# Kernel tuning notes

Measured on AMD Instinct MI355X. Metric: run time of the kernel, lower is better.

Reference implementation:

```python
import jax, jax.numpy as jnp
import numpy as np

# static config (matches init_kwargs)
NH, NKV, E, K = 16, 4, 8, 2
CAP_FACTOR = 1.25
LN_EPS = 1e-5


def _layer_norm(x, w, b):
    mu = jnp.mean(x, axis=-1, keepdims=True)
    var = jnp.mean(jnp.square(x - mu), axis=-1, keepdims=True)
    return (x - mu) * jax.lax.rsqrt(var + LN_EPS) * w + b


def setup_inputs() -> dict:
    key = jax.random.key(0)
    ks = jax.random.split(key, 6)
    S, B, H, F = 2048, 1, 1024, 2048
    HD = H // NH
    qkv_out = NKV * ((NH // NKV) + 2) * HD  # 1536
    f32 = jnp.float32
    return {
        "hidden_states": jax.random.normal(ks[0], (S, B, H), f32),
        "ln1_weight": jnp.ones((H,), f32),
        "ln1_bias": jnp.zeros((H,), f32),
        "ln2_weight": jnp.ones((H,), f32),
        "ln2_bias": jnp.zeros((H,), f32),
        "qkv_weight": jax.random.normal(ks[1], (qkv_out, H), f32) * 0.02,
        "proj_weight": jax.random.normal(ks[2], (H, H), f32) * 0.02,
        "router_weight": jax.random.normal(ks[3], (H, E), f32) * 0.02,
        "moe_w1": jax.random.normal(ks[4], (E, H, F), f32) * 0.02,
        "moe_w2": jax.random.normal(ks[5], (F and E, F, H), f32)[:E] * 0.02 if False else jax.random.normal(ks[5], (E, F, H), f32) * 0.02,
    }


def reference(hidden_states, ln1_weight, ln1_bias, ln2_weight, ln2_bias,
              qkv_weight, proj_weight, router_weight, moe_w1, moe_w2):
    S, B, H = hidden_states.shape
    HD = H // NH
    q_per_kv = NH // NKV
    # ---- attention block (cp_size=1: all-to-alls are identity) ----
    ln1 = _layer_norm(hidden_states, ln1_weight, ln1_bias)
    qkv = jnp.einsum('sbh,oh->sbo', ln1, qkv_weight)
    qkv = qkv.reshape(S, B, NKV, (q_per_kv + 2) * HD)
    q = qkv[..., : q_per_kv * HD].reshape(S, B, NH, HD)
    k = qkv[..., q_per_kv * HD:(q_per_kv + 1) * HD]          # [S,B,NKV,HD]
    v = qkv[..., (q_per_kv + 1) * HD:]                        # [S,B,NKV,HD]
    qb = jnp.transpose(q, (1, 2, 0, 3)).reshape(B, NKV, q_per_kv, S, HD)
    kb = jnp.transpose(k, (1, 2, 0, 3))                       # [B,NKV,S,HD]
    vb = jnp.transpose(v, (1, 2, 0, 3))
    scale = 1.0 / np.sqrt(HD).astype(np.float32)
    scores = jnp.einsum('bgqsd,bgtd->bgqst', qb, kb) * scale  # [B,NKV,qpk,S,S]
    causal = jnp.tril(jnp.ones((S, S), bool))
    scores = jnp.where(causal, scores, jnp.finfo(scores.dtype).min)
    attn = jax.nn.softmax(scores, axis=-1)
    ao = jnp.einsum('bgqst,bgtd->bgqsd', attn, vb)
    ao = ao.reshape(B, NH, S, HD)
    ao = jnp.transpose(ao, (2, 0, 1, 3)).reshape(S, B, H)
    proj = jnp.einsum('sbh,oh->sbo', ao, proj_weight)
    h1 = hidden_states + proj
    # ---- MoE block (ep_size=1: uniform all-to-all is identity) ----
    ln2 = _layer_norm(h1, ln2_weight, ln2_bias)
    x = ln2.reshape(-1, H)                                    # [N,H]
    N = x.shape[0]
    logits = x @ router_weight                                # linear(x, router_weight.t())
    probs = jax.nn.softmax(logits, axis=-1)
    top_p, top_i = jax.lax.top_k(probs, K)
    top_p = top_p / jnp.sum(top_p, axis=-1, keepdims=True)
    exp_idx = top_i.reshape(-1)                               # [N*K]
    exp_p = top_p.reshape(-1)
    # stable sort by expert id, capacity-padded dispatch
    order = jnp.argsort(exp_idx, stable=True)
    sorted_exp = exp_idx[order]
    counts = jnp.bincount(exp_idx, length=E)
    offsets = jnp.concatenate([jnp.zeros((1,), counts.dtype), jnp.cumsum(counts)[:-1]])
    within = jnp.arange(N * K) - offsets[sorted_exp]
    cap = int(np.ceil(N * K / E * CAP_FACTOR))
    T = E * cap
    valid = within < cap
    dst = jnp.where(valid, sorted_exp * cap + within, T)      # T = out-of-bounds -> dropped
    padded_tokens = jnp.zeros((T, H), x.dtype).at[dst].set(x[order // K], mode='drop')
    padded_probs = jnp.zeros((T,), exp_p.dtype).at[dst].set(exp_p[order], mode='drop')
    padded_tid = jnp.zeros((T,), jnp.int32).at[dst].set((order // K).astype(jnp.int32), mode='drop')
    # grouped expert GEMMs: [E,cap,H] x [E,H,F] -> gelu -> [E,cap,H]
    xt = padded_tokens.reshape(E, cap, H)
    fc1 = jax.nn.gelu(jnp.einsum('ech,ehf->ecf', xt, moe_w1))
    fc2 = jnp.einsum('ecf,efh->ech', fc1, moe_w2).reshape(T, H)
    weighted = fc2 * padded_probs[:, None]                    # pad slots have prob 0
    moe_out = jnp.zeros((N, H), hidden_states.dtype).at[padded_tid].add(weighted)
    return h1 + moe_out.reshape(S, B, H)
```

## Files before the change

### kernel.cpp

```cpp
#include <hip/hip_runtime.h>
#include <hip/hip_bf16.h>
#include <stdint.h>

#define S_LEN 2048
#define HDIM  1024
#define NHEAD 16
#define NKVH  4
#define HEADD 64
#define QKV_O 1536
#define NEXP  8
#define TOPK  2
#define CAP   640
#define TCAP  (NEXP*CAP)
#define FDIM  2048
#define LOG2E 1.44269504088896f
#define NCHUNK 40

typedef __bf16 bf16x8 __attribute__((ext_vector_type(8)));
typedef float  f32x4  __attribute__((ext_vector_type(4)));
typedef unsigned int u32;
typedef u32 u32x4 __attribute__((ext_vector_type(4)));
typedef u32 u32x2 __attribute__((ext_vector_type(2)));
typedef unsigned short u16;
typedef u16 u16x8 __attribute__((ext_vector_type(8)));

__device__ __forceinline__ void gload16(const __bf16* g, __bf16* l) {
    __builtin_amdgcn_global_load_lds(
        (const __attribute__((address_space(1))) u32*)g,
        (__attribute__((address_space(3))) u32*)l, 16, 0, 0);
}

__device__ __constant__ const signed char c_strip[NCHUNK] =
    {0,1,2,3, 4,4, 5,5, 6,6, 7,7, 8,8,8, 9,9,9, 10,10,10, 11,11,11,
     12,12,12,12, 13,13,13,13, 14,14,14,14, 15,15,15,15};
__device__ __constant__ const signed char c_chunk[NCHUNK] =
    {0,0,0,0, 0,1, 0,1, 0,1, 0,1, 0,1,2, 0,1,2, 0,1,2, 0,1,2,
     0,1,2,3, 0,1,2,3, 0,1,2,3, 0,1,2,3};
__device__ __constant__ const signed char c_cbase[16] = {0,1,2,3,4,6,8,10,12,15,18,21,24,28,32,36};
__device__ __constant__ const signed char c_nch[16]   = {1,1,1,1,2,2,2,2,3,3,3,3,4,4,4,4};

__global__ __launch_bounds__(256)
void prep_kernel(const float* __restrict__ hidden, const float* __restrict__ ln1w,
                 const float* __restrict__ ln1bb, const float* __restrict__ qkvW,
                 const float* __restrict__ projW, __bf16* __restrict__ ln1o,
                 __bf16* __restrict__ projWb, __bf16* __restrict__ qkvWb) {
    const int b = blockIdx.x, tid = threadIdx.x;
    if (b < S_LEN) {
        __shared__ float red[256];
        const float* x = hidden + (size_t)b * HDIM;
        float xr[4];
        #pragma unroll
        for (int j = 0; j < 4; ++j) xr[j] = x[tid + 256*j];
        float s = xr[0] + xr[1] + xr[2] + xr[3];
        red[tid] = s; __syncthreads();
        for (int st = 128; st > 0; st >>= 1) { if (tid < st) red[tid] += red[tid+st]; __syncthreads(); }
        float mu = red[0] / HDIM; __syncthreads();
        float v = 0.f;
        #pragma unroll
        for (int j = 0; j < 4; ++j) { float d = xr[j]-mu; v += d*d; }
        red[tid] = v; __syncthreads();
        for (int st = 128; st > 0; st >>= 1) { if (tid < st) red[tid] += red[tid+st]; __syncthreads(); }
        float rstd = rsqrtf(red[0]/HDIM + 1e-5f);
        #pragma unroll
        for (int j = 0; j < 4; ++j) {
            int i = tid + 256*j;
            ln1o[(size_t)b*HDIM + i] = (__bf16)((xr[j]-mu)*rstd*ln1w[i] + ln1bb[i]);
        }
        return;
    }
    const float* src; __bf16* dst; int i;
    if (b < S_LEN + 768) { src = qkvW; dst = qkvWb; i = (b - S_LEN)*256 + tid; }
    else                 { src = projW; dst = projWb; i = (b - S_LEN - 768)*256 + tid; }
    const float4* s = (const float4*)src + (size_t)i*2;
    float4 a = s[0], b4 = s[1];
    __bf16 tmp[8] = {(__bf16)a.x,(__bf16)a.y,(__bf16)a.z,(__bf16)a.w,
                     (__bf16)b4.x,(__bf16)b4.y,(__bf16)b4.z,(__bf16)b4.w};
    *(u32x4*)(dst + (size_t)i*8) = *(u32x4*)tmp;
}

__global__ __launch_bounds__(256)
void transp2_kernel(const float* __restrict__ w1, const float* __restrict__ w2,
                    __bf16* __restrict__ w1t, __bf16* __restrict__ w2t) {
    __shared__ float t[64][65];
    const int b = blockIdx.x;
    const float* src; __bf16* dst; int K, N, n0, k0;
    if (b < 4096) {
        int e = b >> 9, rem = b & 511;
        K = HDIM; N = FDIM; n0 = (rem & 31) * 64; k0 = (rem >> 5) * 64;
        src = w1 + (size_t)e*K*N; dst = w1t + (size_t)e*K*N;
    } else {
        int bb = b - 4096; int e = bb >> 9, rem = bb & 511;
        K = FDIM; N = HDIM; n0 = (rem & 15) * 64; k0 = (rem >> 4) * 64;
        src = w2 + (size_t)e*K*N; dst = w2t + (size_t)e*K*N;
    }
    const int tid = threadIdx.x;
    const int r = tid >> 4, c4 = (tid & 15) * 4;
    #pragma unroll
    for (int i = 0; i < 4; ++i) {
        float4 v = *(const float4*)(src + (size_t)(k0 + r + 16*i)*N + n0 + c4);
        t[r+16*i][c4+0] = v.x; t[r+16*i][c4+1] = v.y;
        t[r+16*i][c4+2] = v.z; t[r+16*i][c4+3] = v.w;
    }
    __syncthreads();
    const int rn = tid >> 3, kc = (tid & 7) * 8;
    #pragma unroll
    for (int i = 0; i < 2; ++i) {
        int n = rn + 32*i;
        __bf16 tmp[8];
        #pragma unroll
        for (int j = 0; j < 8; ++j) tmp[j] = (__bf16)t[kc+j][n];
        *(u32x4*)(dst + (size_t)(n0+n)*K + k0 + kc) = *(u32x4*)tmp;
    }
}

template<int EPI>
__global__ __launch_bounds__(256)
void gemm_bf16_kernel(const __bf16* __restrict__ A, const __bf16* __restrict__ Bt,
                      const float* __restrict__ R, void* __restrict__ Cout,
                      int N, int K, long sA, long sB, long sC) {
    __shared__ __bf16 As[128*64];
    __shared__ __bf16 Bs[128*64];
    const int e = blockIdx.z;
    A  += (size_t)e * sA;
    Bt += (size_t)e * sB;
    const int m0 = blockIdx.y*128, n0 = blockIdx.x*128;
    const int tid = threadIdx.x;
    const int lane = tid & 63, w = tid >> 6;
    const int lr = lane & 15, lg = lane >> 4;
    const int wr = w >> 1, wc = w & 1;
    const int srow8 = lane >> 3, sg = lane & 7;
    f32x4 acc[4][4] = {};
    for (int k0 = 0; k0 < K; k0 += 64) {
        __syncthreads();
        #pragma unroll
        for (int i = 0; i < 4; ++i) {
            int row = 32*w + 8*i + srow8;
            int src_g = sg ^ (row & 7);
            gload16(A  + (size_t)(m0+row)*K + k0 + src_g*8,
                    (__bf16*)((char*)As + (32*w + 8*i)*128));
            gload16(Bt + (size_t)(n0+row)*K + k0 + src_g*8,
                    (__bf16*)((char*)Bs + (32*w + 8*i)*128));
        }
        __syncthreads();
        #pragma unroll
        for (int ks = 0; ks < 2; ++ks) {
            bf16x8 af[4], bfr[4];
            #pragma unroll
            for (int mi = 0; mi < 4; ++mi) {
                int row = wr*64 + mi*16 + lr;
                af[mi] = *(const bf16x8*)((const char*)As + ((row*128 + (lg+4*ks)*16) ^ ((row&7)<<4)));
            }
            #pragma unroll
            for (int ni = 0; ni < 4; ++ni) {
                int row = wc*64 + ni*16 + lr;
                bfr[ni] = *(const bf16x8*)((const char*)Bs + ((row*128 + (lg+4*ks)*16) ^ ((row&7)<<4)));
            }
            #pragma unroll
            for (int mi = 0; mi < 4; ++mi)
                #pragma unroll
                for (int ni = 0; ni < 4; ++ni)
                    acc[mi][ni] = __builtin_amdgcn_mfma_f32_16x16x32_bf16(af[mi], bfr[ni], acc[mi][ni], 0,0,0);
        }
    }
    #pragma unroll
    for (int mi = 0; mi < 4; ++mi) {
        #pragma unroll
        for (int ni = 0; ni < 4; ++ni) {
            #pragma unroll
            for (int r = 0; r < 4; ++r) {
                int row = m0 + wr*64 + mi*16 + lg*4 + r;
                int col = n0 + wc*64 + ni*16 + lr;
                float v = acc[mi][ni][r];
                if (EPI == 1) v += R[(size_t)row*N + col];
                if (EPI == 2) {
                    float t = 0.7978845608028654f * (v + 0.044715f*v*v*v);
                    v = 0.5f * v * (1.f + tanhf(t));
                }
                if (EPI == 2 || EPI == 3)
                    ((__bf16*)Cout)[(size_t)e*sC + (size_t)row*N + col] = (__bf16)v;
                else
                    ((float*)Cout)[(size_t)e*sC + (size_t)row*N + col] = v;
            }
        }
    }
}

__global__ __launch_bounds__(512)
void attn_part_kernel(const __bf16* __restrict__ qkv, float* __restrict__ partO,
                      float* __restrict__ partML) {
    const int cx = blockIdx.x;
    const int h  = blockIdx.y;
    const int hg = h >> 2, qi = h & 3;
    const int qb = c_strip[cx];
    const int t0 = 4 * c_chunk[cx];
    const int t1 = min(qb + 1, t0 + 4);
    const int q0 = qb * 128;
    const int tid  = threadIdx.x;
    const int w    = tid >> 6;
    const int lane = tid & 63;
    const int lr   = lane & 15;
    const int lg   = lane >> 4;

    __shared__ __attribute__((aligned(16))) __bf16 Kls[128*64];
    __shared__ __attribute__((aligned(16))) __bf16 Vls[64*128];
    __shared__ __attribute__((aligned(16))) __bf16 Pls[8][16*64];

    const int krow = tid >> 2, kc = (tid & 3) * 2;
    const int va = tid & 63,  dg  = tid >> 6;
    u32x4 kreg[2]; u16x8 vreg[2];

    const __bf16* kbase = qkv + hg*384 + 256;
    const __bf16* vbase = qkv + hg*384 + 320;

#define ISSUE(T) do { \
        const __bf16* kp = kbase + (size_t)((T)*128 + krow)*QKV_O + kc*8; \
        kreg[0] = *(const u32x4*)(kp); \
        kreg[1] = *(const u32x4*)(kp + 8); \
        const __bf16* vp = vbase + (size_t)((T)*128 + 2*va)*QKV_O + dg*8; \
        vreg[0] = *(const u16x8*)(vp); \
        vreg[1] = *(const u16x8*)(vp + QKV_O); \
    } while(0)

#define COMMIT() do { \
        char* Kb = (char*)Kls; \
        *(u32x4*)(Kb + ((krow*128 + (kc+0)*16) ^ ((krow&7)<<4))) = kreg[0]; \
        *(u32x4*)(Kb + ((krow*128 + (kc+1)*16) ^ ((krow&7)<<4))) = kreg[1]; \
        char* Vb = (char*)Vls; \
        _Pragma("unroll") \
        for (int j = 0; j < 8; ++j) { \
            int d = dg*8 + j; \
            u32 u = ((u32)vreg[1][j] << 16) | vreg[0][j]; \
            *(u32*)(Vb + ((d*256 + va*4) ^ ((d&7)<<4))) = u; \
        } \
    } while(0)

    const int qrow = q0 + w*16 + lr;
    const __bf16* qp = qkv + (size_t)qrow*QKV_O + hg*384 + qi*64;
    bf16x8 qfrag[2];
    #pragma unroll
    for (int ks = 0; ks < 2; ++ks) {
        bf16x8 qr = *(const bf16x8*)(qp + ks*32 + lg*8);
        #pragma unroll
        for (int j = 0; j < 8; ++j) qfrag[ks][j] = (__bf16)((float)qr[j] * 0.125f);
    }
    bf16x8 ones;
    #pragma unroll
    for (int j = 0; j < 8; ++j) ones[j] = (__bf16)1.0f;

    f32x4 oacc[4] = {};
    f32x4 lcol = {};
    float mrow[4] = {-INFINITY,-INFINITY,-INFINITY,-INFINITY};

    ISSUE(t0);
    for (int t = t0; t < t1; ++t) {
        __syncthreads();
        COMMIT();
        if (t+1 < t1) ISSUE(t+1);
        __syncthreads();

        f32x4 sacc[8] = {};
        const char* Kb = (const char*)Kls;
        #pragma unroll
        for (int f = 0; f < 8; ++f) {
            int row = lr + 16*f;
            int swz = (row & 7) << 4;
            #pragma unroll
            for (int ks = 0; ks < 2; ++ks) {
                bf16x8 kf = *(const bf16x8*)(Kb + ((row*128 + (lg*8+32*ks)*2) ^ swz));
                sacc[f] = __builtin_amdgcn_mfma_f32_16x16x32_bf16(qfrag[ks], kf, sacc[f], 0,0,0);
            }
        }
        if (t == qb) {
            #pragma unroll
            for (int f = 0; f < 8; ++f)
                #pragma unroll
                for (int r = 0; r < 4; ++r)
                    if (lr + 16*f > 16*w + 4*lg + r) sacc[f][r] = -INFINITY;
        }
        float tm[4];
        #pragma unroll
        for (int r = 0; r < 4; ++r) {
            float a = fmaxf(fmaxf(sacc[0][r], sacc[1][r]), fmaxf(sacc[2][r], sacc[3][r]));
            float b2 = fmaxf(fmaxf(sacc[4][r], sacc[5][r]), fmaxf(sacc[6][r], sacc[7][r]));
            tm[r] = fmaxf(a, b2);
        }
        #pragma unroll
        for (int msk = 1; msk < 16; msk <<= 1)
            #pragma unroll
            for (int r = 0; r < 4; ++r) tm[r] = fmaxf(tm[r], __shfl_xor(tm[r], msk, 64));
        float corr[4];
        #pragma unroll
        for (int r = 0; r < 4; ++r) {
            float mn = fmaxf(mrow[r], tm[r]);
            corr[r] = exp2f((mrow[r]-mn)*LOG2E);
            mrow[r] = mn;
        }
        #pragma unroll
        for (int f = 0; f < 8; ++f)
            #pragma unroll
            for (int r = 0; r < 4; ++r)
                sacc[f][r] = exp2f((sacc[f][r]-mrow[r])*LOG2E);
        #pragma unroll
        for (int ct = 0; ct < 4; ++ct)
            #pragma unroll
            for (int r = 0; r < 4; ++r) oacc[ct][r] *= corr[r];
        #pragma unroll
        for (int r = 0; r < 4; ++r) lcol[r] *= corr[r];

        char* Pw = (char*)&Pls[w][0];
        const char* Vb = (const char*)Vls;
        #pragma unroll
        for (int half = 0; half < 2; ++half) {
            #pragma unroll
            for (int f = 0; f < 4; ++f)
                #pragma unroll
                for (int r = 0; r < 4; ++r) {
                    int row = 4*lg + r, col = lr + 16*f;
                    *(__bf16*)(Pw + ((row*128 + col*2) ^ ((row&7)<<4))) = (__bf16)sacc[4*half+f][r];
                }
            bf16x8 pa[2];
            #pragma unroll
            for (int ks = 0; ks < 2; ++ks)
                pa[ks] = *(const bf16x8*)(Pw + ((lr*128 + (lg*8+32*ks)*2) ^ ((lr&7)<<4)));
            #pragma unroll
            for (int ks = 0; ks < 2; ++ks)
                lcol = __builtin_amdgcn_mfma_f32_16x16x32_bf16(pa[ks], ones, lcol, 0,0,0);
            #pragma unroll
            for (int ct = 0; ct < 4; ++ct) {
                int row = lr + 16*ct;
                int swz = (row & 7) << 4;
                #pragma unroll
                for (int ks = 0; ks < 2; ++ks) {
                    int gks = 2*half + ks;
                    bf16x8 vf = *(const bf16x8*)(Vb + ((row*256 + (lg*8+32*gks)*2) ^ swz));
                    oacc[ct] = __builtin_amdgcn_mfma_f32_16x16x32_bf16(pa[ks], vf, oacc[ct], 0,0,0);
                }
            }
        }
    }
    const int p = h*NCHUNK + cx;
    float* po = partO + (size_t)p * (128*64);
    #pragma unroll
    for (int ct = 0; ct < 4; ++ct)
        #pragma unroll
        for (int r = 0; r < 4; ++r)
            po[(16*w + 4*lg + r)*64 + 16*ct + lr] = oacc[ct][r];
    if (lr == 0) {
        float* pm = partML + (size_t)p * 256;
        #pragma unroll
        for (int r = 0; r < 4; ++r) {
            pm[(16*w + 4*lg + r)*2    ] = mrow[r];
            pm[(16*w + 4*lg + r)*2 + 1] = lcol[r];
        }
    }
#undef ISSUE
#undef COMMIT
}

__global__ __launch_bounds__(256)
void attn_combine_kernel(const float* __restrict__ partO, const float* __restrict__ partML,
                         __bf16* __restrict__ ao) {
    const int rb = blockIdx.x, h = blockIdx.y;
    const int row0 = rb*8;
    const int qb = row0 >> 7;
    const int nc = c_nch[qb], cb = c_cbase[qb];
    const int tid = threadIdx.x;
    const int rl = tid >> 5, d2 = (tid & 31) * 2;
    const int grow = row0 + rl;
    const int srow = grow & 127;
    const int pbase = h*NCHUNK + cb;
    float mv[4], lv[4];
    float M = -INFINITY;
    for (int c = 0; c < nc; ++c) {
        const float* pm = partML + (size_t)(pbase+c)*256 + srow*2;
        mv[c] = pm[0]; lv[c] = pm[1];
        M = fmaxf(M, mv[c]);
    }
    float L = 0.f, a0 = 0.f, a1 = 0.f;
    for (int c = 0; c < nc; ++c) {
        float wc = exp2f((mv[c]-M)*LOG2E);
        L += wc * lv[c];
        const float* po = partO + (size_t)(pbase+c)*(128*64) + srow*64 + d2;
        a0 += wc * po[0];
        a1 += wc * po[1];
    }
    float inv = 1.f / L;
    __bf16 o2[2] = {(__bf16)(a0*inv), (__bf16)(a1*inv)};
    *(u32*)(ao + (size_t)grow*HDIM + h*64 + d2) = *(u32*)o2;
}

__global__ __launch_bounds__(256)
void ln2_router_kernel(const float* __restrict__ h1, const float* __restrict__ w,
                       const float* __restrict__ b, const float* __restrict__ rw,
                       __bf16* __restrict__ x2b, int* __restrict__ expi,
                       float* __restrict__ expp) {
    const int t = blockIdx.x, tid = threadIdx.x;
    __shared__ float red[256];
    __shared__ float red8[256][8];
    const float* x = h1 + (size_t)t*HDIM;
    float xr[4];
    #pragma unroll
    for (int j = 0; j < 4; ++j) xr[j] = x[tid + 256*j];
    float s = xr[0] + xr[1] + xr[2] + xr[3];
    red[tid] = s; __syncthreads();
    for (int st = 128; st > 0; st >>= 1) { if (tid < st) red[tid] += red[tid+st]; __syncthreads(); }
    float mu = red[0] / HDIM; __syncthreads();
    float v = 0.f;
    #pragma unroll
    for (int j = 0; j < 4; ++j) { float d = xr[j]-mu; v += d*d; }
    red[tid] = v; __syncthreads();
    for (int st = 128; st > 0; st >>= 1) { if (tid < st) red[tid] += red[tid+st]; __syncthreads(); }
    float rstd = rsqrtf(red[0]/HDIM + 1e-5f);
    float part[8] = {};
    #pragma unroll
    for (int j = 0; j < 4; ++j) {
        int i = tid + 256*j;
        float o = (xr[j]-mu)*rstd*w[i] + b[i];
        x2b[(size_t)t*HDIM + i] = (__bf16)o;
        const float* wp = rw + (size_t)i*NEXP;
        #pragma unroll
        for (int e2 = 0; e2 < 8; ++e2) part[e2] += o * wp[e2];
    }
    #pragma unroll
    for (int e2 = 0; e2 < 8; ++e2) red8[tid][e2] = part[e2];
    __syncthreads();
    for (int st = 128; st > 0; st >>= 1) {
        if (tid < st)
            #pragma unroll
            for (int e2 = 0; e2 < 8; ++e2) red8[tid][e2] += red8[tid+st][e2];
        __syncthreads();
    }
    if (tid == 0) {
        float lg[8];
        #pragma unroll
        for (int e2 = 0; e2 < 8; ++e2) lg[e2] = red8[0][e2];
        int i0 = 0;
        for (int e2 = 1; e2 < 8; ++e2) if (lg[e2] > lg[i0]) i0 = e2;
        int i1 = -1;
        for (int e2 = 0; e2 < 8; ++e2) { if (e2 == i0) continue; if (i1 < 0 || lg[e2] > lg[i1]) i1 = e2; }
        float p1 = __expf(lg[i1] - lg[i0]);
        float inv = 1.f / (1.f + p1);
        expi[t*2]   = i0; expi[t*2+1] = i1;
        expp[t*2]   = inv; expp[t*2+1] = p1 * inv;
    }
}

__global__ __launch_bounds__(256)
void dst_fast_kernel(const int* __restrict__ expi, int* __restrict__ dst) {
    __shared__ int hist[256][9];
    const int tid = threadIdx.x;
    int ev[16];
    #pragma unroll
    for (int i = 0; i < 16; i += 4)
        *(int4*)(ev+i) = *(const int4*)(expi + tid*16 + i);
    int cnt[8] = {};
    #pragma unroll
    for (int i = 0; i < 16; ++i)
        #pragma unroll
        for (int e = 0; e < 8; ++e) cnt[e] += (ev[i] == e);
    #pragma unroll
    for (int e = 0; e < 8; ++e) hist[tid][e] = cnt[e];
    __syncthreads();
    const int w = tid >> 6, lane = tid & 63;
    #pragma unroll
    for (int rep = 0; rep < 2; ++rep) {
        int e = w + rep*4;
        int h0 = hist[4*lane+0][e], h1 = hist[4*lane+1][e],
            h2 = hist[4*lane+2][e], h3 = hist[4*lane+3][e];
        int s = h0+h1+h2+h3, inc = s;
        #pragma unroll
        for (int off = 1; off < 64; off <<= 1) {
            int v = __shfl_up(inc, off, 64);
            if (lane >= off) inc += v;
        }
        int excl = inc - s;
        hist[4*lane+0][e] = excl;
        hist[4*lane+1][e] = excl + h0;
        hist[4*lane+2][e] = excl + h0 + h1;
        hist[4*lane+3][e] = excl + h0 + h1 + h2;
    }
    __syncthreads();
    int run[8];
    #pragma unroll
    for (int e = 0; e < 8; ++e) run[e] = hist[tid][e];
    int out[16];
    #pragma unroll
    for (int i = 0; i < 16; ++i) {
        int e = ev[i], within = 0;
        #pragma unroll
        for (int e2 = 0; e2 < 8; ++e2)
            if (e == e2) { within = run[e2]; run[e2]++; }
        out[i] = (within < CAP) ? (e*CAP + within) : -1;
    }
    #pragma unroll
    for (int i = 0; i < 16; i += 4)
        *(int4*)(dst + tid*16 + i) = *(const int4*)(out+i);
}

__global__ void scatter_kernel(const __bf16* __restrict__ x2b, const int* __restrict__ dst,
                               __bf16* __restrict__ xt) {
    int s = blockIdx.x;
    int d = dst[s];
    if (d < 0) return;
    int t = s >> 1;
    int i = threadIdx.x;
    u32x2 v = *(const u32x2*)(x2b + (size_t)t*HDIM + i*4);
    *(u32x2*)(xt + (size_t)d*HDIM + i*4) = v;
}

__global__ void combine_kernel(const float* __restrict__ h1, const float* __restrict__ fc2,
                               const int* __restrict__ dst, const float* __restrict__ expp,
                               float* __restrict__ out) {
    int t = blockIdx.x;
    int d0 = dst[t*2], d1 = dst[t*2+1];
    float p0 = expp[t*2], p1 = expp[t*2+1];
    int i = threadIdx.x * 4;
    float4 v = *(const float4*)(h1 + (size_t)t*HDIM + i);
    if (d0 >= 0) {
        float4 f = *(const float4*)(fc2 + (size_t)d0*HDIM + i);
        v.x += p0*f.x; v.y += p0*f.y; v.z += p0*f.z; v.w += p0*f.w;
    }
    if (d1 >= 0) {
        float4 f = *(const float4*)(fc2 + (size_t)d1*HDIM + i);
        v.x += p1*f.x; v.y += p1*f.y; v.z += p1*f.z; v.w += p1*f.w;
    }
    *(float4*)(out + (size_t)t*HDIM + i) = v;
}

extern "C" void kernel_launch(void* const* d_in, const int* in_sizes, int n_in,
                              void* d_out, int out_size, void* d_ws, size_t ws_size,
                              hipStream_t stream) {
    const float* hidden = (const float*)d_in[0];
    const float* ln1w   = (const float*)d_in[1];
    const float* ln1b_  = (const float*)d_in[2];
    const float* ln2w   = (const float*)d_in[3];
    const float* ln2b_  = (const float*)d_in[4];
    const float* qkvW   = (const float*)d_in[5];
    const float* projW  = (const float*)d_in[6];
    const float* routW  = (const float*)d_in[7];
    const float* w1     = (const float*)d_in[8];
    const float* w2     = (const float*)d_in[9];
    float* out = (float*)d_out;

    char* base = (char*)d_ws;
    __bf16* w1t    = (__bf16*)(base);
    __bf16* w2t    = (__bf16*)(base + 33554432);
    __bf16* ln1b   = (__bf16*)(base + 0);
    __bf16* qkvWb  = (__bf16*)(base + 4194304);
    __bf16* qkvb   = (__bf16*)(base + 7340032);
    __bf16* aob    = (__bf16*)(base + 13631488);
    __bf16* projWb = (__bf16*)(base + 17825792);
    char* B0 = base + 67108864;
    float*  h1   = (float*)(B0);
    __bf16* xtb  = (__bf16*)(B0 + 8388608);
    __bf16* fc1b = (__bf16*)(B0 + 18874368);
    float*  fc2  = (float*)(B0 + 39845888);
    __bf16* x2b  = (__bf16*)fc2;
    int*    expi = (int*)(B0 + 60817408);
    int*    dsts = (int*)(B0 + 60833792);
    float*  expp = (float*)(B0 + 60850176);
    float*  partML = (float*)xtb;
    float*  partO  = (float*)fc1b;

    prep_kernel<<<S_LEN + 768 + 512, 256, 0, stream>>>(
        hidden, ln1w, ln1b_, qkvW, projW, ln1b, projWb, qkvWb);
    gemm_bf16_kernel<3><<<dim3(QKV_O/128, S_LEN/128, 1), 256, 0, stream>>>(
        ln1b, qkvWb, nullptr, qkvb, QKV_O, HDIM, 0, 0, 0);
    attn_part_kernel<<<dim3(NCHUNK, NHEAD), 512, 0, stream>>>(qkvb, partO, partML);
    attn_combine_kernel<<<dim3(S_LEN/8, NHEAD), 256, 0, stream>>>(partO, partML, aob);
    gemm_bf16_kernel<1><<<dim3(HDIM/128, S_LEN/128, 1), 256, 0, stream>>>(
        aob, projWb, hidden, h1, HDIM, HDIM, 0, 0, 0);
    ln2_router_kernel<<<S_LEN, 256, 0, stream>>>(h1, ln2w, ln2b_, routW, x2b, expi, expp);
    dst_fast_kernel<<<1, 256, 0, stream>>>(expi, dsts);
    scatter_kernel<<<S_LEN*TOPK, 256, 0, stream>>>(x2b, dsts, xtb);
    transp2_kernel<<<8192, 256, 0, stream>>>(w1, w2, w1t, w2t);
    gemm_bf16_kernel<2><<<dim3(FDIM/128, CAP/128, NEXP), 256, 0, stream>>>(
        xtb, w1t, nullptr, fc1b, FDIM, HDIM,
        (long)CAP*HDIM, (long)FDIM*HDIM, (long)CAP*FDIM);
    gemm_bf16_kernel<0><<<dim3(HDIM/128, CAP/128, NEXP), 256, 0, stream>>>(
        fc1b, w2t, nullptr, fc2, HDIM, FDIM,
        (long)CAP*FDIM, (long)FDIM*HDIM, (long)CAP*HDIM);
    combine_kernel<<<S_LEN, 256, 0, stream>>>(h1, fc2, dsts, expp, out);
}
```

Before: 250.4 us.

## Fuse expert weight transpose into attention launch as extra blocks

Removes the standalone transp2 launch. Its tiles now run as extra blocks, two tiles per 512-thread block, appended to the attention kernel's grid. The goal is to overlap the memory-bound fp32-to-bf16 transpose of the MoE weights with the compute-bound attention partial kernel, which has only 640 blocks. To avoid the transposed weights overwriting live data, the qkv, attention-output and proj-weight buffers move into the fc2 scratch region. Shared memory is unified into one 48KB buffer, which may change attention occupancy. The overlap depends on how the scheduler interleaves the two kinds of blocks.

```diff
diff --git a/kernel.cpp b/kernel.cpp
--- a/kernel.cpp
+++ b/kernel.cpp
@@ -15,6 +15,8 @@
 #define FDIM  2048
 #define LOG2E 1.44269504088896f
 #define NCHUNK 40
+#define ATTN_BLOCKS (NCHUNK*NHEAD)
+#define TRANSP_BLOCKS 4096
 
 typedef __bf16 bf16x8 __attribute__((ext_vector_type(8)));
 typedef float  f32x4  __attribute__((ext_vector_type(4)));
@@ -76,41 +78,6 @@
     __bf16 tmp[8] = {(__bf16)a.x,(__bf16)a.y,(__bf16)a.z,(__bf16)a.w,
                      (__bf16)b4.x,(__bf16)b4.y,(__bf16)b4.z,(__bf16)b4.w};
     *(u32x4*)(dst + (size_t)i*8) = *(u32x4*)tmp;
-}
-
-__global__ __launch_bounds__(256)
-void transp2_kernel(const float* __restrict__ w1, const float* __restrict__ w2,
-                    __bf16* __restrict__ w1t, __bf16* __restrict__ w2t) {
-    __shared__ float t[64][65];
-    const int b = blockIdx.x;
-    const float* src; __bf16* dst; int K, N, n0, k0;
-    if (b < 4096) {
-        int e = b >> 9, rem = b & 511;
-        K = HDIM; N = FDIM; n0 = (rem & 31) * 64; k0 = (rem >> 5) * 64;
-        src = w1 + (size_t)e*K*N; dst = w1t + (size_t)e*K*N;
-    } else {
-        int bb = b - 4096; int e = bb >> 9, rem = bb & 511;
-        K = FDIM; N = HDIM; n0 = (rem & 15) * 64; k0 = (rem >> 4) * 64;
-        src = w2 + (size_t)e*K*N; dst = w2t + (size_t)e*K*N;
-    }
-    const int tid = threadIdx.x;
-    const int r = tid >> 4, c4 = (tid & 15) * 4;
-    #pragma unroll
-    for (int i = 0; i < 4; ++i) {
-        float4 v = *(const float4*)(src + (size_t)(k0 + r + 16*i)*N + n0 + c4);
-        t[r+16*i][c4+0] = v.x; t[r+16*i][c4+1] = v.y;
-        t[r+16*i][c4+2] = v.z; t[r+16*i][c4+3] = v.w;
-    }
-    __syncthreads();
-    const int rn = tid >> 3, kc = (tid & 7) * 8;
-    #pragma unroll
-    for (int i = 0; i < 2; ++i) {
-        int n = rn + 32*i;
-        __bf16 tmp[8];
-        #pragma unroll
-        for (int j = 0; j < 8; ++j) tmp[j] = (__bf16)t[kc+j][n];
-        *(u32x4*)(dst + (size_t)(n0+n)*K + k0 + kc) = *(u32x4*)tmp;
-    }
 }
 
 template<int EPI>
@@ -186,10 +153,51 @@
 }
 
 __global__ __launch_bounds__(512)
-void attn_part_kernel(const __bf16* __restrict__ qkv, float* __restrict__ partO,
-                      float* __restrict__ partML) {
-    const int cx = blockIdx.x;
-    const int h  = blockIdx.y;
+void attn_transp_kernel(const __bf16* __restrict__ qkv, float* __restrict__ partO,
+                        float* __restrict__ partML,
+                        const float* __restrict__ w1, const float* __restrict__ w2,
+                        __bf16* __restrict__ w1t, __bf16* __restrict__ w2t) {
+    __shared__ __attribute__((aligned(16))) char smem[49152];
+    const int bid = blockIdx.x;
+
+    if (bid >= ATTN_BLOCKS) {
+        const int half = threadIdx.x >> 8, t256 = threadIdx.x & 255;
+        float (*t)[65] = (float(*)[65])(smem + half*16640);
+        const int tile = (bid - ATTN_BLOCKS)*2 + half;
+        const float* src; __bf16* dst; int K, N, n0, k0;
+        if (tile < 4096) {
+            int e = tile >> 9, rem = tile & 511;
+            K = HDIM; N = FDIM; n0 = (rem & 31) * 64; k0 = (rem >> 5) * 64;
+            src = w1 + (size_t)e*K*N; dst = w1t + (size_t)e*K*N;
+        } else {
+            int tt = tile - 4096; int e = tt >> 9, rem = tt & 511;
+            K = FDIM; N = HDIM; n0 = (rem & 15) * 64; k0 = (rem >> 4) * 64;
+            src = w2 + (size_t)e*K*N; dst = w2t + (size_t)e*K*N;
+        }
+        const int r = t256 >> 4, c4 = (t256 & 15) * 4;
+        #pragma unroll
+        for (int i = 0; i < 4; ++i) {
+            float4 v = *(const float4*)(src + (size_t)(k0 + r + 16*i)*N + n0 + c4);
+            t[r+16*i][c4+0] = v.x; t[r+16*i][c4+1] = v.y;
+            t[r+16*i][c4+2] = v.z; t[r+16*i][c4+3] = v.w;
+        }
+        __syncthreads();
+        const int rn = t256 >> 3, kc = (t256 & 7) * 8;
+        #pragma unroll
+        for (int i = 0; i < 2; ++i) {
+            int n = rn + 32*i;
+            __bf16 tmp[8];
+            #pragma unroll
+            for (int j = 0; j < 8; ++j) tmp[j] = (__bf16)t[kc+j][n];
+            *(u32x4*)(dst + (size_t)(n0+n)*K + k0 + kc) = *(u32x4*)tmp;
+        }
+        return;
+    }
+
+    __bf16* Kls = (__bf16*)smem;
+    __bf16* Vls = (__bf16*)(smem + 16384);
+    const int cx = bid % NCHUNK;
+    const int h  = bid / NCHUNK;
     const int hg = h >> 2, qi = h & 3;
     const int qb = c_strip[cx];
     const int t0 = 4 * c_chunk[cx];
@@ -200,10 +208,6 @@
     const int lane = tid & 63;
     const int lr   = lane & 15;
     const int lg   = lane >> 4;
-
-    __shared__ __attribute__((aligned(16))) __bf16 Kls[128*64];
-    __shared__ __attribute__((aligned(16))) __bf16 Vls[64*128];
-    __shared__ __attribute__((aligned(16))) __bf16 Pls[8][16*64];
 
     const int krow = tid >> 2, kc = (tid & 3) * 2;
     const int va = tid & 63,  dg  = tid >> 6;
@@ -307,7 +311,7 @@
         #pragma unroll
         for (int r = 0; r < 4; ++r) lcol[r] *= corr[r];
 
-        char* Pw = (char*)&Pls[w][0];
+        char* Pw = smem + 32768 + w*2048;
         const char* Vb = (const char*)Vls;
         #pragma unroll
         for (int half = 0; half < 2; ++half) {
@@ -545,17 +549,17 @@
     char* base = (char*)d_ws;
     __bf16* w1t    = (__bf16*)(base);
     __bf16* w2t    = (__bf16*)(base + 33554432);
-    __bf16* ln1b   = (__bf16*)(base + 0);
+    __bf16* ln1b   = (__bf16*)(base);
     __bf16* qkvWb  = (__bf16*)(base + 4194304);
-    __bf16* qkvb   = (__bf16*)(base + 7340032);
-    __bf16* aob    = (__bf16*)(base + 13631488);
-    __bf16* projWb = (__bf16*)(base + 17825792);
     char* B0 = base + 67108864;
     float*  h1   = (float*)(B0);
     __bf16* xtb  = (__bf16*)(B0 + 8388608);
     __bf16* fc1b = (__bf16*)(B0 + 18874368);
     float*  fc2  = (float*)(B0 + 39845888);
-    __bf16* x2b  = (__bf16*)fc2;
+    __bf16* x2b    = (__bf16*)fc2;
+    __bf16* qkvb   = (__bf16*)((char*)fc2 + 4194304);
+    __bf16* aob    = (__bf16*)((char*)fc2 + 10485760);
+    __bf16* projWb = (__bf16*)((char*)fc2 + 14680064);
     int*    expi = (int*)(B0 + 60817408);
     int*    dsts = (int*)(B0 + 60833792);
     float*  expp = (float*)(B0 + 60850176);
@@ -566,14 +570,14 @@
         hidden, ln1w, ln1b_, qkvW, projW, ln1b, projWb, qkvWb);
     gemm_bf16_kernel<3><<<dim3(QKV_O/128, S_LEN/128, 1), 256, 0, stream>>>(
         ln1b, qkvWb, nullptr, qkvb, QKV_O, HDIM, 0, 0, 0);
-    attn_part_kernel<<<dim3(NCHUNK, NHEAD), 512, 0, stream>>>(qkvb, partO, partML);
+    attn_transp_kernel<<<ATTN_BLOCKS + TRANSP_BLOCKS, 512, 0, stream>>>(
+        qkvb, partO, partML, w1, w2, w1t, w2t);
     attn_combine_kernel<<<dim3(S_LEN/8, NHEAD), 256, 0, stream>>>(partO, partML, aob);
     gemm_bf16_kernel<1><<<dim3(HDIM/128, S_LEN/128, 1), 256, 0, stream>>>(
         aob, projWb, hidden, h1, HDIM, HDIM, 0, 0, 0);
     ln2_router_kernel<<<S_LEN, 256, 0, stream>>>(h1, ln2w, ln2b_, routW, x2b, expi, expp);
     dst_fast_kernel<<<1, 256, 0, stream>>>(expi, dsts);
     scatter_kernel<<<S_LEN*TOPK, 256, 0, stream>>>(x2b, dsts, xtb);
-    transp2_kernel<<<8192, 256, 0, stream>>>(w1, w2, w1t, w2t);
     gemm_bf16_kernel<2><<<dim3(FDIM/128, CAP/128, NEXP), 256, 0, stream>>>(
         xtb, w1t, nullptr, fc1b, FDIM, HDIM,
         (long)CAP*HDIM, (long)FDIM*HDIM, (long)CAP*FDIM);
```

After: 244.8 us. 1.02x faster.
